# Kernel optimization log

Hardware: AMD Instinct MI355X
Metric: run time of the kernel (lower is better)

## Reference

```python
import jax, jax.numpy as jnp
import numpy as np

D_MODEL = 256
D_STATE = 64
HEADDIM = 64
EXPAND = 2
D_INNER = EXPAND * D_MODEL        # 512
D_SSM = D_INNER                   # 512
NGROUPS = 1
NHEADS = D_SSM // HEADDIM         # 8
CONV_DIM = D_SSM + 2 * NGROUPS * D_STATE   # 640
D_IN_PROJ = 2 * D_INNER + 2 * NGROUPS * D_STATE + NHEADS  # 1160
BATCH, Himg, Wimg = 8, 64, 64
EPS = 1e-5


def causal_dw_conv1d(x, w, b):
    """Depthwise causal conv1d + SiLU. x:(B,C,L), w:(C,K), b:(C,)"""
    K = w.shape[1]
    L = x.shape[-1]
    xp = jnp.pad(x, ((0, 0), (0, 0), (K - 1, 0)))
    y = b[None, :, None]
    for k in range(K):
        y = y + w[:, k][None, :, None] * xp[:, :, k:k + L]
    return jax.nn.silu(y)


def setup_inputs() -> dict:
    key = jax.random.key(0)
    ks = jax.random.split(key, 12)
    u = jax.random.normal(ks[0], (BATCH, D_MODEL, Himg, Wimg), jnp.float32)
    in_proj_w = jax.random.normal(ks[1], (D_IN_PROJ, D_MODEL), jnp.float32) * 0.02
    conv_dt_w = jax.random.normal(ks[2], (NHEADS, 4), jnp.float32) * 0.1
    # dt_bias via inverse-softplus of dt ~ logU(1e-3, 0.1) as in the module init
    dt0 = jnp.exp(jax.random.uniform(ks[3], (NHEADS,)) * (np.log(0.1) - np.log(0.001)) + np.log(0.001))
    dt_bias = dt0 + jnp.log(-jnp.expm1(-dt0))
    conv_xBC_w = jax.random.normal(ks[4], (CONV_DIM, 3), jnp.float32) * 0.1
    conv_xBC_b = jax.random.normal(ks[5], (CONV_DIM,), jnp.float32) * 0.02
    conv_z_w = jax.random.normal(ks[6], (D_SSM, 3), jnp.float32) * 0.1
    conv_z_b = jax.random.normal(ks[7], (D_SSM,), jnp.float32) * 0.02
    A_log = jnp.log(jax.random.uniform(ks[8], (NHEADS,), minval=1.0, maxval=16.0))
    D_param = jnp.ones((NHEADS,), jnp.float32)
    norm_w = jnp.ones((D_SSM,), jnp.float32)
    out_proj_w = jax.random.normal(ks[9], (D_MODEL, D_SSM, 3, 3), jnp.float32) * 0.02
    return {"u": u, "in_proj_w": in_proj_w, "conv_dt_w": conv_dt_w, "dt_bias": dt_bias,
            "conv_xBC_w": conv_xBC_w, "conv_xBC_b": conv_xBC_b,
            "conv_z_w": conv_z_w, "conv_z_b": conv_z_b,
            "A_log": A_log, "D_param": D_param, "norm_w": norm_w, "out_proj_w": out_proj_w}


def reference(u, in_proj_w, conv_dt_w, dt_bias, conv_xBC_w, conv_xBC_b,
              conv_z_w, conv_z_b, A_log, D_param, norm_w, out_proj_w):
    B, C, H, W = u.shape
    L = H * W
    # 1x1 conv in_proj -> (B, D_IN_PROJ, L)
    zxbcdt = jnp.einsum('oc,bchw->bohw', in_proj_w, u).reshape(B, D_IN_PROJ, L)
    z = zxbcdt[:, :D_SSM]                                  # (B, D_SSM, L)
    xBC = zxbcdt[:, D_SSM:D_SSM + CONV_DIM]                # (B, CONV_DIM, L)
    dt = zxbcdt[:, D_SSM + CONV_DIM:]                      # (B, NHEADS, L)

    A = -jnp.exp(A_log)                                    # (NHEADS,)
    dt = causal_dw_conv1d(dt, conv_dt_w, dt_bias)          # (B, H, L), silu'd
    xBC = causal_dw_conv1d(xBC, conv_xBC_w, conv_xBC_b)    # (B, CONV_DIM, L)

    x = xBC[:, :D_SSM]                                     # (B, D_SSM, L)
    Bm = jnp.transpose(xBC[:, D_SSM:D_SSM + D_STATE], (0, 2, 1))   # (B, L, N)
    Cm = jnp.transpose(xBC[:, D_SSM + D_STATE:], (0, 2, 1))        # (B, L, N)

    # x: (B, h*c, L) -> V: (B, h, L, c)
    V = jnp.transpose(x.reshape(B, NHEADS, HEADDIM, L), (0, 1, 3, 2))
    # dA = dt * A per head: (B, h, L, 1)
    dA = dt[:, :, :, None] * A[None, :, None, None]
    V_scaled = V * dA
    # non-causal linear attention duality (ngroups==1)
    KV = jnp.einsum('bln,bhld->bhnd', Bm, V_scaled)        # (B, h, N, d)
    y = jnp.einsum('bln,bhnd->bhld', Cm, KV) + V * D_param[None, :, None, None]
    y = jnp.transpose(y, (0, 2, 1, 3)).reshape(B, L, D_SSM)

    # gate branch
    zc = causal_dw_conv1d(z, conv_z_w, conv_z_b)           # (B, D_SSM, L)
    zc = jnp.transpose(zc, (0, 2, 1))                      # (B, L, D_SSM)
    # RMSNormGated, norm_before_gate=False: gate first then normalize
    yg = y * jax.nn.silu(zc)
    yn = yg * jax.lax.rsqrt(jnp.mean(yg * yg, axis=-1, keepdims=True) + EPS) * norm_w

    y_img = jnp.transpose(yn, (0, 2, 1)).reshape(B, D_SSM, H, W)
    out = jax.lax.conv_general_dilated(y_img, out_proj_w, (1, 1), 'SAME',
                                       dimension_numbers=('NCHW', 'OIHW', 'NCHW'))
    return out
```

## Files before the change

kernel.cpp:

```cpp
#include <hip/hip_runtime.h>
#include <math.h>


constexpr int BATCH  = 8;
constexpr int CIN    = 256;
constexpr int HH     = 64, WW = 64;
constexpr int L      = HH * WW;
constexpr int DPROJ  = 1160;
constexpr int DSSM   = 512;
constexpr int DSTATE = 64;
constexpr int NH     = 8;
constexpr int HD     = 64;
constexpr int CONVD  = 640;
constexpr int COUT   = 256;
constexpr float EPS  = 1e-5f;

typedef __attribute__((ext_vector_type(8))) short short8;
typedef __attribute__((ext_vector_type(4))) float f32x4;

static __device__ __forceinline__ float silu_f(float x) {
    return x / (1.f + __expf(-x));
}
static __device__ __forceinline__ float bf2f(unsigned short u) {
    return __uint_as_float(((unsigned)u) << 16);
}
static __device__ __forceinline__ unsigned short f2bf(float f) {
    unsigned x = __float_as_uint(f);
    unsigned r = (x + 0x7FFFu + ((x >> 16) & 1u)) >> 16;
    return (unsigned short)r;
}

static __device__ __forceinline__ void gl2lds16(const unsigned short* g, short* l) {
    __builtin_amdgcn_global_load_lds(
        (const __attribute__((address_space(1))) unsigned int*)g,
        (__attribute__((address_space(3))) unsigned int*)l, 16, 0, 0);
}

__global__ __launch_bounds__(256) void k_prep(const float* __restrict__ W,
                                              const float* __restrict__ u,
                                              const float* __restrict__ Wt,
                                              unsigned short* __restrict__ Wt2,
                                              unsigned short* __restrict__ uTt,
                                              unsigned short* __restrict__ Wb2) {
    __shared__ float Ts[32][33];
    int bx = blockIdx.x;
    int tid = threadIdx.x;

    if (bx < 160) {
        int idx8 = bx * 256 + tid;
        int tile = idx8 >> 9;
        int within = (idx8 & 511) * 8;
        int row = within >> 5;
        int slp = (within >> 3) & 3;
        int oblk = tile >> 3, ks = tile & 7;
        int o = oblk * 128 + row;
        int c = ks * 32 + (slp ^ (row & 3)) * 8;
        unsigned short s[8] = {0, 0, 0, 0, 0, 0, 0, 0};
        if (o < DPROJ) {
            float4 v0 = *(const float4*)(W + (size_t)o * CIN + c);
            float4 v1 = *(const float4*)(W + (size_t)o * CIN + c + 4);
            s[0] = f2bf(v0.x); s[1] = f2bf(v0.y); s[2] = f2bf(v0.z); s[3] = f2bf(v0.w);
            s[4] = f2bf(v1.x); s[5] = f2bf(v1.y); s[6] = f2bf(v1.z); s[7] = f2bf(v1.w);
        }
        *(uint4*)(Wt2 + (size_t)tile * 4096 + within) = *(uint4*)s;
    } else if (bx < 160 + 8192) {
        int t = bx - 160;
        int l0 = (t & 127) * 32;
        int c0 = ((t >> 7) & 7) * 32;
        int b  = t >> 10;
        {
            int r = tid >> 3, c4 = tid & 7;
            float4 v = *(const float4*)(u + ((size_t)b * CIN + c0 + r) * L + l0 + c4 * 4);
            Ts[r][c4 * 4 + 0] = v.x;
            Ts[r][c4 * 4 + 1] = v.y;
            Ts[r][c4 * 4 + 2] = v.z;
            Ts[r][c4 * 4 + 3] = v.w;
        }
        __syncthreads();
        {
            int lr = tid >> 3, cg = tid & 7;
            unsigned short s[4];
#pragma unroll
            for (int j = 0; j < 4; ++j) s[j] = f2bf(Ts[cg * 4 + j][lr]);
            int lg = l0 + lr;
            int tile = ((b * 32 + (lg >> 7)) << 3) + (c0 >> 5);
            int row = lg & 127;
            int slot = (cg >> 1) ^ (row & 3);
            size_t off = (size_t)tile * 4096 + row * 32 + slot * 8 + (cg & 1) * 4;
            *(uint2*)(uTt + off) = *(uint2*)s;
        }
    } else {
        int i = (bx - (160 + 8192)) * 256 + tid;
        int co = i >> 9, ci = i & 511;
        const float* src = Wt + (size_t)i * 9;
#pragma unroll
        for (int tap = 0; tap < 9; ++tap) {
            Wb2[(((size_t)tap * 64 + (ci >> 3)) * 256 + co) * 8 + (ci & 7)] = f2bf(src[tap]);
        }
    }
}

__global__ __launch_bounds__(256) void k_inprojm(const unsigned short* __restrict__ Wt2,
                                                 const unsigned short* __restrict__ uTt,
                                                 unsigned short* __restrict__ zx) {
    __shared__ short Ab[2][4096];
    __shared__ short Bbuf[2][4096];
    int lblk = blockIdx.x, oblk = blockIdx.y, b = blockIdx.z;
    int tid = threadIdx.x, lane = tid & 63, w = tid >> 6;
    int laneN = lane & 15, laneK = lane >> 4;

    const unsigned short* At = uTt + (size_t)(b * 32 + lblk) * 8 * 4096;
    const unsigned short* Bt = Wt2 + (size_t)oblk * 8 * 4096;

    f32x4 acc[4][4];
#pragma unroll
    for (int mt = 0; mt < 4; ++mt)
#pragma unroll
        for (int nt = 0; nt < 4; ++nt) acc[mt][nt] = (f32x4){0.f, 0.f, 0.f, 0.f};

    gl2lds16(At + tid * 8,        &Ab[0][tid * 8]);
    gl2lds16(At + 2048 + tid * 8, &Ab[0][2048 + tid * 8]);
    gl2lds16(Bt + tid * 8,        &Bbuf[0][tid * 8]);
    gl2lds16(Bt + 2048 + tid * 8, &Bbuf[0][2048 + tid * 8]);
    __syncthreads();

    int arow = (w & 1) * 64;
    int brow = (w >> 1) * 64;
    int asl = (laneK ^ (laneN & 3)) * 8;

    int cur = 0;
    for (int ks = 0; ks < 8; ++ks) {
        if (ks < 7) {
            const unsigned short* an = At + (size_t)(ks + 1) * 4096;
            const unsigned short* bn = Bt + (size_t)(ks + 1) * 4096;
            int c2 = cur ^ 1;
            gl2lds16(an + tid * 8,        &Ab[c2][tid * 8]);
            gl2lds16(an + 2048 + tid * 8, &Ab[c2][2048 + tid * 8]);
            gl2lds16(bn + tid * 8,        &Bbuf[c2][tid * 8]);
            gl2lds16(bn + 2048 + tid * 8, &Bbuf[c2][2048 + tid * 8]);
        }
        short8 av[4], bv[4];
#pragma unroll
        for (int mt = 0; mt < 4; ++mt)
            av[mt] = *(const short8*)&Ab[cur][(arow + mt * 16 + laneN) * 32 + asl];
#pragma unroll
        for (int nt = 0; nt < 4; ++nt)
            bv[nt] = *(const short8*)&Bbuf[cur][(brow + nt * 16 + laneN) * 32 + asl];
#pragma unroll
        for (int mt = 0; mt < 4; ++mt)
#pragma unroll
            for (int nt = 0; nt < 4; ++nt)
                acc[mt][nt] = __builtin_amdgcn_mfma_f32_16x16x32_bf16(av[mt], bv[nt], acc[mt][nt], 0, 0, 0);
        __syncthreads();
        cur ^= 1;
    }

    unsigned short* zb = zx + (size_t)b * DPROJ * L;
    int lbase = lblk * 128 + arow;
#pragma unroll
    for (int nt = 0; nt < 4; ++nt) {
        int o = oblk * 128 + brow + nt * 16 + laneN;
        if (o < DPROJ) {
#pragma unroll
            for (int mt = 0; mt < 4; ++mt) {
                unsigned short s[4] = {f2bf(acc[mt][nt].x), f2bf(acc[mt][nt].y),
                                       f2bf(acc[mt][nt].z), f2bf(acc[mt][nt].w)};
                *(uint2*)(zb + (size_t)o * L + lbase + mt * 16 + laneK * 4) = *(uint2*)s;
            }
        }
    }
}

__global__ __launch_bounds__(256) void k_conv1(const unsigned short* __restrict__ zx,
                                               const float* __restrict__ cw,
                                               const float* __restrict__ cb,
                                               const float* __restrict__ dw,
                                               const float* __restrict__ db,
                                               const float* __restrict__ Alog,
                                               unsigned short* __restrict__ xbc,
                                               float* __restrict__ dA) {
    int bx = blockIdx.x;
    int tid = threadIdx.x;
    if (bx < 10240) {
        int idx = bx * 256 + tid;
        int lg = idx & (L / 8 - 1);
        int c  = (idx >> 9) % CONVD;
        int b  = idx / (CONVD * (L / 8));
        int l0 = lg * 8;
        const unsigned short* row = zx + ((size_t)b * DPROJ + DSSM + c) * L;
        float x[10];
        uint4 raw = *(const uint4*)(row + l0);
        const unsigned short* s = (const unsigned short*)&raw;
#pragma unroll
        for (int t = 0; t < 8; ++t) x[2 + t] = bf2f(s[t]);
        if (l0 > 0) { x[0] = bf2f(row[l0 - 2]); x[1] = bf2f(row[l0 - 1]); }
        else        { x[0] = 0.f; x[1] = 0.f; }
        float w0 = cw[c * 3 + 0], w1 = cw[c * 3 + 1], w2 = cw[c * 3 + 2], bb = cb[c];
        uint4 o;
        unsigned short* os = (unsigned short*)&o;
#pragma unroll
        for (int t = 0; t < 8; ++t) {
            float y = bb + w0 * x[t] + w1 * x[t + 1] + w2 * x[t + 2];
            os[t] = f2bf(silu_f(y));
        }
        *(uint4*)(xbc + ((size_t)b * CONVD + c) * L + l0) = o;
    } else {
        int idx = (bx - 10240) * 256 + tid;
        int l = idx & (L - 1);
        int h = (idx >> 12) & (NH - 1);
        int b = idx >> 15;
        const unsigned short* row = zx + ((size_t)b * DPROJ + DSSM + CONVD + h) * L;
        float y = db[h];
#pragma unroll
        for (int k = 0; k < 4; ++k) {
            int ls = l + k - 3;
            if (ls >= 0) y += dw[h * 4 + k] * bf2f(row[ls]);
        }
        dA[idx] = silu_f(y) * (-__expf(Alog[h]));
    }
}

__global__ __launch_bounds__(256) void k_kvm(const unsigned short* __restrict__ xbc,
                                             const float* __restrict__ dA,
                                             float* __restrict__ pKV) {
    __shared__ float red[4][4096];
    int kc = blockIdx.x, h = blockIdx.y, b = blockIdx.z;
    int tid = threadIdx.x, lane = tid & 63, w = tid >> 6;
    int laneN = lane & 15, laneK = lane >> 4;

    const unsigned short* Bb = xbc + ((size_t)b * CONVD + DSSM) * L;
    const unsigned short* Vb = xbc + ((size_t)b * CONVD + h * HD) * L;
    const float* dAp = dA + ((size_t)b * NH + h) * L;

    f32x4 acc[4][4];
#pragma unroll
    for (int mt = 0; mt < 4; ++mt)
#pragma unroll
        for (int nt = 0; nt < 4; ++nt) acc[mt][nt] = (f32x4){0.f, 0.f, 0.f, 0.f};

    int kbase = kc * 512 + w * 128;
#pragma unroll
    for (int ks = 0; ks < 4; ++ks) {
        int kl = kbase + ks * 32 + laneK * 8;
        float4 da0 = *(const float4*)(dAp + kl);
        float4 da1 = *(const float4*)(dAp + kl + 4);
        float dav[8] = {da0.x, da0.y, da0.z, da0.w, da1.x, da1.y, da1.z, da1.w};
        short8 afr[4];
#pragma unroll
        for (int mt = 0; mt < 4; ++mt) {
            uint4 raw = *(const uint4*)(Bb + (size_t)(mt * 16 + laneN) * L + kl);
            const unsigned short* s = (const unsigned short*)&raw;
            short8 af;
#pragma unroll
            for (int j = 0; j < 8; ++j) af[j] = (short)f2bf(bf2f(s[j]) * dav[j]);
            afr[mt] = af;
        }
#pragma unroll
        for (int nt = 0; nt < 4; ++nt) {
            short8 bfr = *(const short8*)(Vb + (size_t)(nt * 16 + laneN) * L + kl);
#pragma unroll
            for (int mt = 0; mt < 4; ++mt)
                acc[mt][nt] = __builtin_amdgcn_mfma_f32_16x16x32_bf16(afr[mt], bfr, acc[mt][nt], 0, 0, 0);
        }
    }

#pragma unroll
    for (int mt = 0; mt < 4; ++mt)
#pragma unroll
        for (int nt = 0; nt < 4; ++nt)
#pragma unroll
            for (int j = 0; j < 4; ++j)
                red[w][(mt * 16 + laneK * 4 + j) * 64 + nt * 16 + laneN] = acc[mt][nt][j];
    __syncthreads();

    float* dst = pKV + (((size_t)(b * NH + h) * 8 + kc) * 4096);
#pragma unroll
    for (int q = 0; q < 4; ++q) {
        int off = q * 1024 + tid * 4;
        float4 s0 = *(const float4*)&red[0][off];
        float4 s1 = *(const float4*)&red[1][off];
        float4 s2 = *(const float4*)&red[2][off];
        float4 s3 = *(const float4*)&red[3][off];
        float4 r;
        r.x = s0.x + s1.x + s2.x + s3.x;
        r.y = s0.y + s1.y + s2.y + s3.y;
        r.z = s0.z + s1.z + s2.z + s3.z;
        r.w = s0.w + s1.w + s2.w + s3.w;
        *(float4*)(dst + off) = r;
    }
}

__global__ __launch_bounds__(256) void k_kvred(const float* __restrict__ pKV,
                                               float* __restrict__ KV) {
    int flat4 = blockIdx.x * 256 + threadIdx.x;
    int bh = flat4 >> 10;
    int nd = (flat4 & 1023) * 4;
    float4 r = make_float4(0.f, 0.f, 0.f, 0.f);
#pragma unroll
    for (int kc = 0; kc < 8; ++kc) {
        float4 v = *(const float4*)(pKV + ((size_t)bh * 8 + kc) * 4096 + nd);
        r.x += v.x; r.y += v.y; r.z += v.z; r.w += v.w;
    }
    *(float4*)(KV + (size_t)bh * 4096 + nd) = r;
}

constexpr int Y_LT = 128;

__global__ __launch_bounds__(256) void k_y5a(const unsigned short* __restrict__ xbc,
                                             const unsigned short* __restrict__ zx,
                                             const float* __restrict__ KV,
                                             const float* __restrict__ zw,
                                             const float* __restrict__ zb,
                                             const float* __restrict__ Dp,
                                             unsigned short* __restrict__ ygout) {
    __shared__ float Cs[DSTATE][Y_LT + 4];
    __shared__ float KVs[DSTATE][HD + 4];
    int l0 = blockIdx.x * Y_LT;
    int h  = blockIdx.y;
    int b  = blockIdx.z;
    int tid = threadIdx.x;
    int td = tid >> 4, tl = tid & 15;

    const unsigned short* xb = xbc + (size_t)b * CONVD * L;
#pragma unroll
    for (int j = 0; j < 4; ++j) {
        int i = j * 256 + tid;
        int nn = i >> 4, c8 = i & 15;
        uint4 raw = *(const uint4*)(xb + (size_t)(DSSM + DSTATE + nn) * L + l0 + c8 * 8);
        const unsigned short* s = (const unsigned short*)&raw;
#pragma unroll
        for (int t = 0; t < 8; ++t) Cs[nn][c8 * 8 + t] = bf2f(s[t]);
    }
    const float* kvb = KV + ((size_t)b * NH + h) * DSTATE * HD;
#pragma unroll
    for (int j = 0; j < 4; ++j) {
        int i = j * 256 + tid;
        int nn = i >> 4, d4 = i & 15;
        *(float4*)&KVs[nn][d4 * 4] = *(const float4*)(kvb + (size_t)nn * HD + d4 * 4);
    }
    __syncthreads();

    float acc[4][8];
#pragma unroll
    for (int i = 0; i < 4; ++i)
#pragma unroll
        for (int j = 0; j < 8; ++j) acc[i][j] = 0.f;

    for (int nn = 0; nn < DSTATE; ++nn) {
        float4 kv = *(const float4*)&KVs[nn][td * 4];
        float cl[8];
        *(float4*)&cl[0] = *(const float4*)&Cs[nn][tl * 8];
        *(float4*)&cl[4] = *(const float4*)&Cs[nn][tl * 8 + 4];
#pragma unroll
        for (int j = 0; j < 8; ++j) {
            acc[0][j] += kv.x * cl[j];
            acc[1][j] += kv.y * cl[j];
            acc[2][j] += kv.z * cl[j];
            acc[3][j] += kv.w * cl[j];
        }
    }

    float Dh = Dp[h];
    int lbase = l0 + tl * 8;
#pragma unroll
    for (int dj = 0; dj < 4; ++dj) {
        int c = h * HD + td * 4 + dj;
        float v[8];
        {
            uint4 raw = *(const uint4*)(xb + (size_t)c * L + lbase);
            const unsigned short* s = (const unsigned short*)&raw;
#pragma unroll
            for (int t = 0; t < 8; ++t) v[t] = bf2f(s[t]);
        }
        const unsigned short* zrow = zx + ((size_t)b * DPROJ + c) * L;
        float zv[12];
        if (lbase >= 4) {
            uint2 z0 = *(const uint2*)(zrow + lbase - 4);
            const unsigned short* s = (const unsigned short*)&z0;
#pragma unroll
            for (int t = 0; t < 4; ++t) zv[t] = bf2f(s[t]);
        } else {
            zv[0] = zv[1] = zv[2] = zv[3] = 0.f;
        }
        {
            uint4 z1 = *(const uint4*)(zrow + lbase);
            const unsigned short* s = (const unsigned short*)&z1;
#pragma unroll
            for (int t = 0; t < 8; ++t) zv[4 + t] = bf2f(s[t]);
        }
        float w0 = zw[c * 3 + 0], w1 = zw[c * 3 + 1], w2 = zw[c * 3 + 2];
        float bz = zb[c];
        uint4 pk;
        unsigned short* sp = (unsigned short*)&pk;
#pragma unroll
        for (int lj = 0; lj < 8; ++lj) {
            float y = acc[dj][lj] + v[lj] * Dh;
            float zy = bz + w0 * zv[lj + 2] + w1 * zv[lj + 3] + w2 * zv[lj + 4];
            sp[lj] = f2bf(y * silu_f(silu_f(zy)));
        }
        *(uint4*)(ygout + (size_t)b * DPROJ * L + (size_t)c * L + lbase) = pk;
    }
}

constexpr int R_LT = 32;

__global__ __launch_bounds__(256) void k_y5bT(const unsigned short* __restrict__ yg,
                                              const float* __restrict__ nw,
                                              unsigned short* __restrict__ ynT) {
    __shared__ float ygs[DSSM][R_LT + 1];
    __shared__ float red[8][R_LT];
    __shared__ float rs[R_LT];
    int l0 = blockIdx.x * R_LT;
    int b  = blockIdx.y;
    int tid = threadIdx.x;
    int ll = tid & 31, grp = tid >> 5;
    const unsigned short* ygb = yg + (size_t)b * DPROJ * L;
#pragma unroll
    for (int j = 0; j < 8; ++j) {
        int i = j * 256 + tid;
        int c = i >> 2, q = i & 3;
        uint4 raw = *(const uint4*)(ygb + (size_t)c * L + l0 + q * 8);
        const unsigned short* s = (const unsigned short*)&raw;
#pragma unroll
        for (int t = 0; t < 8; ++t) ygs[c][q * 8 + t] = bf2f(s[t]);
    }
    __syncthreads();
    float ss = 0.f;
#pragma unroll
    for (int ci = 0; ci < 64; ++ci) {
        float t = ygs[grp * 64 + ci][ll];
        ss += t * t;
    }
    red[grp][ll] = ss;
    __syncthreads();
    if (tid < R_LT) {
        float s = 0.f;
#pragma unroll
        for (int g = 0; g < 8; ++g) s += red[g][tid];
        rs[tid] = rsqrtf(s * (1.f / DSSM) + EPS);
    }
    __syncthreads();
    int lc = tid & 31, cg = tid >> 5;
    float r = rs[lc];
    unsigned short* dst = ynT + ((size_t)b * L + l0 + lc) * DSSM + cg * 64;
#pragma unroll
    for (int j = 0; j < 8; ++j) {
        uint4 pk;
        unsigned short* sp = (unsigned short*)&pk;
#pragma unroll
        for (int t = 0; t < 8; ++t) {
            int c = cg * 64 + j * 8 + t;
            sp[t] = f2bf(ygs[c][lc] * r * nw[c]);
        }
        *(uint4*)(dst + j * 8) = pk;
    }
}

__global__ __launch_bounds__(256, 4) void k_conv3m(const unsigned short* __restrict__ ynT,
                                                   const unsigned short* __restrict__ Wb2,
                                                   float* __restrict__ out) {
    __shared__ short Alds[4 * 66 * 72];
    int h0  = blockIdx.x * 2;
    int co0 = blockIdx.y * 64;
    int b   = blockIdx.z;
    int tid  = threadIdx.x;
    int lane = tid & 63;
    int wid  = tid >> 6;
    int wm = wid >> 1, wn = wid & 1;
    int laneN = lane & 15, laneK = lane >> 4;

    f32x4 acc[4][2];
#pragma unroll
    for (int mt = 0; mt < 4; ++mt)
#pragma unroll
        for (int nt = 0; nt < 2; ++nt) acc[mt][nt] = (f32x4){0.f, 0.f, 0.f, 0.f};

    const unsigned short* ynb = ynT + (size_t)b * L * DSSM;

    const int a_wi1 = tid >> 2, a_sl = tid & 3;

    if (tid < 64) {
        int rw = tid >> 3, q = tid & 7;
        int r = rw >> 1, wi = (rw & 1) ? 65 : 0;
        *(uint4*)&Alds[(r * 66 + wi) * 72 + q * 8] = make_uint4(0u, 0u, 0u, 0u);
    }

    uint4 pA[8];
#pragma unroll
    for (int j = 0; j < 4; ++j) {
        int hrow = h0 - 1 + j;
        bool ok = (hrow >= 0 && hrow < HH);
        const unsigned short* src = ynb + (size_t)(hrow * WW + a_wi1) * DSSM;
#pragma unroll
        for (int s2 = 0; s2 < 2; ++s2) {
            pA[j * 2 + s2] = make_uint4(0u, 0u, 0u, 0u);
            if (ok) pA[j * 2 + s2] = *(const uint4*)(src + (a_sl + s2 * 4) * 8);
        }
    }

    const unsigned short* wbp =
        Wb2 + ((size_t)laneK * 256 + co0 + wn * 32 + laneN) * 8;

    for (int ci0 = 0; ci0 < DSSM; ci0 += 64) {
        __syncthreads();
#pragma unroll
        for (int j = 0; j < 4; ++j)
#pragma unroll
            for (int s2 = 0; s2 < 2; ++s2)
                *(uint4*)&Alds[(j * 66 + a_wi1 + 1) * 72 + (a_sl + s2 * 4) * 8] = pA[j * 2 + s2];
        __syncthreads();

        if (ci0 + 64 < DSSM) {
            int cin = ci0 + 64;
#pragma unroll
            for (int j = 0; j < 4; ++j) {
                int hrow = h0 - 1 + j;
                bool ok = (hrow >= 0 && hrow < HH);
                const unsigned short* src = ynb + (size_t)(hrow * WW + a_wi1) * DSSM + cin;
#pragma unroll
                for (int s2 = 0; s2 < 2; ++s2) {
                    pA[j * 2 + s2] = make_uint4(0u, 0u, 0u, 0u);
                    if (ok) pA[j * 2 + s2] = *(const uint4*)(src + (a_sl + s2 * 4) * 8);
                }
            }
        }

        const unsigned short* wbc = wbp + (size_t)(ci0 >> 3) * 2048;
        short8 bC[4];
#pragma unroll
        for (int ks = 0; ks < 2; ++ks)
#pragma unroll
            for (int nt = 0; nt < 2; ++nt)
                bC[ks * 2 + nt] = *(const short8*)(wbc + (size_t)ks * 8192 + nt * 128);
#pragma unroll
        for (int tap = 0; tap < 9; ++tap) {
            short8 bN[4];
#pragma unroll
            for (int q = 0; q < 4; ++q) bN[q] = bC[q];
            if (tap < 8) {
#pragma unroll
                for (int ks = 0; ks < 2; ++ks)
#pragma unroll
                    for (int nt = 0; nt < 2; ++nt)
                        bN[ks * 2 + nt] = *(const short8*)(wbc + (size_t)(tap + 1) * 131072 +
                                                          (size_t)ks * 8192 + nt * 128);
            }
            const int kh = tap / 3, kw = tap % 3;
#pragma unroll
            for (int ks = 0; ks < 2; ++ks) {
#pragma unroll
                for (int mt = 0; mt < 4; ++mt) {
                    short8 af = *(const short8*)&Alds[((wm + kh) * 66 + laneN + mt * 16 + kw) * 72 +
                                                      (laneK + ks * 4) * 8];
                    acc[mt][0] = __builtin_amdgcn_mfma_f32_16x16x32_bf16(af, bC[ks * 2 + 0], acc[mt][0], 0, 0, 0);
                    acc[mt][1] = __builtin_amdgcn_mfma_f32_16x16x32_bf16(af, bC[ks * 2 + 1], acc[mt][1], 0, 0, 0);
                }
            }
#pragma unroll
            for (int q = 0; q < 4; ++q) bC[q] = bN[q];
        }
    }

    float* ob = out + (size_t)b * COUT * L + (size_t)(h0 + wm) * WW;
#pragma unroll
    for (int mt = 0; mt < 4; ++mt) {
#pragma unroll
        for (int nt = 0; nt < 2; ++nt) {
            int co = co0 + wn * 32 + nt * 16 + laneN;
            float4 v = make_float4(acc[mt][nt].x, acc[mt][nt].y, acc[mt][nt].z, acc[mt][nt].w);
            *(float4*)(ob + (size_t)co * L + mt * 16 + laneK * 4) = v;
        }
    }
}

extern "C" void kernel_launch(void* const* d_in, const int* in_sizes, int n_in,
                              void* d_out, int out_size, void* d_ws, size_t ws_size,
                              hipStream_t stream) {
    const float* u          = (const float*)d_in[0];
    const float* in_proj_w  = (const float*)d_in[1];
    const float* conv_dt_w  = (const float*)d_in[2];
    const float* dt_bias    = (const float*)d_in[3];
    const float* conv_xBC_w = (const float*)d_in[4];
    const float* conv_xBC_b = (const float*)d_in[5];
    const float* conv_z_w   = (const float*)d_in[6];
    const float* conv_z_b   = (const float*)d_in[7];
    const float* A_log      = (const float*)d_in[8];
    const float* D_param    = (const float*)d_in[9];
    const float* norm_w     = (const float*)d_in[10];
    const float* out_w      = (const float*)d_in[11];
    float* out = (float*)d_out;

    const size_t n_zx  = (size_t)BATCH * DPROJ * L;
    const size_t n_xbc = (size_t)BATCH * CONVD * L;
    const size_t n_yn  = (size_t)BATCH * DSSM * L;
    const size_t n_dA  = (size_t)BATCH * NH * L;
    const size_t n_KV  = (size_t)BATCH * NH * DSTATE * HD;
    const size_t n_pKV = (size_t)BATCH * NH * 8 * DSTATE * HD;
    const size_t n_Wb2 = (size_t)9 * 64 * 256 * 8;
    const size_t need  = 2 * (n_zx + n_xbc + n_yn + n_Wb2) + 4 * (n_dA + n_KV + n_pKV);
    if (ws_size < need) return;

    unsigned short* zx  = (unsigned short*)d_ws;
    unsigned short* xbc = zx + n_zx;
    unsigned short* ynT = xbc + n_xbc;
    float*          dAb = (float*)(ynT + n_yn);
    float*          KV  = dAb + n_dA;
    float*          pKV = KV + n_KV;
    unsigned short* Wb2 = (unsigned short*)(pKV + n_pKV);
    unsigned short* uTt  = ynT;
    unsigned short* Wt2  = (unsigned short*)pKV;
    unsigned short* ygbuf = zx + (size_t)DSSM * L;

    k_prep<<<8864, 256, 0, stream>>>(in_proj_w, u, out_w, Wt2, uTt, Wb2);

    dim3 g1(L / 128, 10, BATCH);
    k_inprojm<<<g1, 256, 0, stream>>>(Wt2, uTt, zx);

    k_conv1<<<11264, 256, 0, stream>>>(zx, conv_xBC_w, conv_xBC_b,
                                       conv_dt_w, dt_bias, A_log, xbc, dAb);

    dim3 g4(8, NH, BATCH);
    k_kvm<<<g4, 256, 0, stream>>>(xbc, dAb, pKV);
    k_kvred<<<256, 256, 0, stream>>>(pKV, KV);

    dim3 g5(L / Y_LT, NH, BATCH);
    k_y5a<<<g5, 256, 0, stream>>>(xbc, zx, KV, conv_z_w, conv_z_b, D_param, ygbuf);

    dim3 g5b(L / R_LT, BATCH);
    k_y5bT<<<g5b, 256, 0, stream>>>(ygbuf, norm_w, ynT);

    dim3 g6(HH / 2, COUT / 64, BATCH);
    k_conv3m<<<g6, 256, 0, stream>>>(ynT, Wb2, out);
}
```

Baseline: 238.9 us.

## Switch output 3x3 conv to 32x32x16 MFMA with 128-channel output tiles

Rewrites the final 3x3 convolution GEMM to use 32x32x16 bf16 MFMA instructions instead of 16x16x32, and doubles the output-channel tile per block from 64 to 128. The weight prep layout changes to 16-element K groups to match the new operand layout. Larger tiles halve redundant reloads of the activation halo into LDS and improve math density per LDS read. In exchange, accumulator registers grow and launch bounds drop to 2 blocks per SM, with half as many blocks in the grid.

Result: slower. 255.3 us (+6.8%).

```diff
diff --git a/kernel.cpp b/kernel.cpp
--- a/kernel.cpp
+++ b/kernel.cpp
@@ -15,8 +15,9 @@
 constexpr int COUT   = 256;
 constexpr float EPS  = 1e-5f;
 
-typedef __attribute__((ext_vector_type(8))) short short8;
-typedef __attribute__((ext_vector_type(4))) float f32x4;
+typedef __attribute__((ext_vector_type(8)))  short short8;
+typedef __attribute__((ext_vector_type(4)))  float f32x4;
+typedef __attribute__((ext_vector_type(16))) float f32x16;
 
 static __device__ __forceinline__ float silu_f(float x) {
     return x / (1.f + __expf(-x));
@@ -41,7 +42,7 @@
                                               const float* __restrict__ Wt,
                                               unsigned short* __restrict__ Wt2,
                                               unsigned short* __restrict__ uTt,
-                                              unsigned short* __restrict__ Wb2) {
+                                              unsigned short* __restrict__ Wb3) {
     __shared__ float Ts[32][33];
     int bx = blockIdx.x;
     int tid = threadIdx.x;
@@ -95,7 +96,7 @@
         const float* src = Wt + (size_t)i * 9;
 #pragma unroll
         for (int tap = 0; tap < 9; ++tap) {
-            Wb2[(((size_t)tap * 64 + (ci >> 3)) * 256 + co) * 8 + (ci & 7)] = f2bf(src[tap]);
+            Wb3[(((size_t)tap * 32 + (ci >> 4)) * 256 + co) * 16 + (ci & 15)] = f2bf(src[tap]);
         }
     }
 }
@@ -456,24 +457,26 @@
     }
 }
 
-__global__ __launch_bounds__(256, 4) void k_conv3m(const unsigned short* __restrict__ ynT,
-                                                   const unsigned short* __restrict__ Wb2,
+__global__ __launch_bounds__(256, 2) void k_conv3m(const unsigned short* __restrict__ ynT,
+                                                   const unsigned short* __restrict__ Wb3,
                                                    float* __restrict__ out) {
     __shared__ short Alds[4 * 66 * 72];
     int h0  = blockIdx.x * 2;
-    int co0 = blockIdx.y * 64;
+    int co0 = blockIdx.y * 128;
     int b   = blockIdx.z;
     int tid  = threadIdx.x;
     int lane = tid & 63;
     int wid  = tid >> 6;
     int wm = wid >> 1, wn = wid & 1;
-    int laneN = lane & 15, laneK = lane >> 4;
-
-    f32x4 acc[4][2];
-#pragma unroll
-    for (int mt = 0; mt < 4; ++mt)
-#pragma unroll
-        for (int nt = 0; nt < 2; ++nt) acc[mt][nt] = (f32x4){0.f, 0.f, 0.f, 0.f};
+    int lane32 = lane & 31, khalf = lane >> 5;
+
+    f32x16 acc[2][2];
+#pragma unroll
+    for (int mt = 0; mt < 2; ++mt)
+#pragma unroll
+        for (int nt = 0; nt < 2; ++nt)
+#pragma unroll
+            for (int q = 0; q < 16; ++q) acc[mt][nt][q] = 0.f;
 
     const unsigned short* ynb = ynT + (size_t)b * L * DSSM;
 
@@ -499,7 +502,7 @@
     }
 
     const unsigned short* wbp =
-        Wb2 + ((size_t)laneK * 256 + co0 + wn * 32 + laneN) * 8;
+        Wb3 + ((size_t)(co0 + wn * 64 + lane32) * 16) + khalf * 8;
 
     for (int ci0 = 0; ci0 < DSSM; ci0 += 64) {
         __syncthreads();
@@ -525,50 +528,59 @@
             }
         }
 
-        const unsigned short* wbc = wbp + (size_t)(ci0 >> 3) * 2048;
-        short8 bC[4];
-#pragma unroll
-        for (int ks = 0; ks < 2; ++ks)
+        const unsigned short* wbc = wbp + (size_t)(ci0 >> 4) * 4096;
+        short8 bC[2][4], bN[2][4];
+#pragma unroll
+        for (int nt = 0; nt < 2; ++nt)
+#pragma unroll
+            for (int ks = 0; ks < 4; ++ks)
+                bC[nt][ks] = *(const short8*)(wbc + (size_t)ks * 4096 + nt * 512);
+#pragma unroll
+        for (int tap = 0; tap < 9; ++tap) {
 #pragma unroll
             for (int nt = 0; nt < 2; ++nt)
-                bC[ks * 2 + nt] = *(const short8*)(wbc + (size_t)ks * 8192 + nt * 128);
-#pragma unroll
-        for (int tap = 0; tap < 9; ++tap) {
-            short8 bN[4];
-#pragma unroll
-            for (int q = 0; q < 4; ++q) bN[q] = bC[q];
+#pragma unroll
+                for (int ks = 0; ks < 4; ++ks) bN[nt][ks] = bC[nt][ks];
             if (tap < 8) {
 #pragma unroll
-                for (int ks = 0; ks < 2; ++ks)
-#pragma unroll
-                    for (int nt = 0; nt < 2; ++nt)
-                        bN[ks * 2 + nt] = *(const short8*)(wbc + (size_t)(tap + 1) * 131072 +
-                                                          (size_t)ks * 8192 + nt * 128);
+                for (int nt = 0; nt < 2; ++nt)
+#pragma unroll
+                    for (int ks = 0; ks < 4; ++ks)
+                        bN[nt][ks] = *(const short8*)(wbc + (size_t)(tap + 1) * 131072 +
+                                                     (size_t)ks * 4096 + nt * 512);
             }
             const int kh = tap / 3, kw = tap % 3;
 #pragma unroll
-            for (int ks = 0; ks < 2; ++ks) {
-#pragma unroll
-                for (int mt = 0; mt < 4; ++mt) {
-                    short8 af = *(const short8*)&Alds[((wm + kh) * 66 + laneN + mt * 16 + kw) * 72 +
-                                                      (laneK + ks * 4) * 8];
-                    acc[mt][0] = __builtin_amdgcn_mfma_f32_16x16x32_bf16(af, bC[ks * 2 + 0], acc[mt][0], 0, 0, 0);
-                    acc[mt][1] = __builtin_amdgcn_mfma_f32_16x16x32_bf16(af, bC[ks * 2 + 1], acc[mt][1], 0, 0, 0);
+            for (int ks = 0; ks < 4; ++ks) {
+#pragma unroll
+                for (int mt = 0; mt < 2; ++mt) {
+                    int wi = mt * 32 + lane32 + kw;
+                    short8 af = *(const short8*)&Alds[((wm + kh) * 66 + wi) * 72 +
+                                                      ks * 16 + khalf * 8];
+                    acc[mt][0] = __builtin_amdgcn_mfma_f32_32x32x16_bf16(af, bC[0][ks], acc[mt][0], 0, 0, 0);
+                    acc[mt][1] = __builtin_amdgcn_mfma_f32_32x32x16_bf16(af, bC[1][ks], acc[mt][1], 0, 0, 0);
                 }
             }
 #pragma unroll
-            for (int q = 0; q < 4; ++q) bC[q] = bN[q];
+            for (int nt = 0; nt < 2; ++nt)
+#pragma unroll
+                for (int ks = 0; ks < 4; ++ks) bC[nt][ks] = bN[nt][ks];
         }
     }
 
     float* ob = out + (size_t)b * COUT * L + (size_t)(h0 + wm) * WW;
 #pragma unroll
-    for (int mt = 0; mt < 4; ++mt) {
+    for (int mt = 0; mt < 2; ++mt) {
 #pragma unroll
         for (int nt = 0; nt < 2; ++nt) {
-            int co = co0 + wn * 32 + nt * 16 + laneN;
-            float4 v = make_float4(acc[mt][nt].x, acc[mt][nt].y, acc[mt][nt].z, acc[mt][nt].w);
-            *(float4*)(ob + (size_t)co * L + mt * 16 + laneK * 4) = v;
+            int co = co0 + wn * 64 + nt * 32 + lane32;
+            float* dst = ob + (size_t)co * L + mt * 32 + 4 * khalf;
+#pragma unroll
+            for (int q = 0; q < 4; ++q) {
+                float4 v = make_float4(acc[mt][nt][q * 4 + 0], acc[mt][nt][q * 4 + 1],
+                                       acc[mt][nt][q * 4 + 2], acc[mt][nt][q * 4 + 3]);
+                *(float4*)(dst + q * 8) = v;
+            }
         }
     }
 }
@@ -596,8 +608,8 @@
     const size_t n_dA  = (size_t)BATCH * NH * L;
     const size_t n_KV  = (size_t)BATCH * NH * DSTATE * HD;
     const size_t n_pKV = (size_t)BATCH * NH * 8 * DSTATE * HD;
-    const size_t n_Wb2 = (size_t)9 * 64 * 256 * 8;
-    const size_t need  = 2 * (n_zx + n_xbc + n_yn + n_Wb2) + 4 * (n_dA + n_KV + n_pKV);
+    const size_t n_Wb3 = (size_t)9 * 32 * 256 * 16;
+    const size_t need  = 2 * (n_zx + n_xbc + n_yn + n_Wb3) + 4 * (n_dA + n_KV + n_pKV);
     if (ws_size < need) return;
 
     unsigned short* zx  = (unsigned short*)d_ws;
@@ -606,12 +618,12 @@
     float*          dAb = (float*)(ynT + n_yn);
     float*          KV  = dAb + n_dA;
     float*          pKV = KV + n_KV;
-    unsigned short* Wb2 = (unsigned short*)(pKV + n_pKV);
+    unsigned short* Wb3 = (unsigned short*)(pKV + n_pKV);
     unsigned short* uTt  = ynT;
     unsigned short* Wt2  = (unsigned short*)pKV;
     unsigned short* ygbuf = zx + (size_t)DSSM * L;
 
-    k_prep<<<8864, 256, 0, stream>>>(in_proj_w, u, out_w, Wt2, uTt, Wb2);
+    k_prep<<<8864, 256, 0, stream>>>(in_proj_w, u, out_w, Wt2, uTt, Wb3);
 
     dim3 g1(L / 128, 10, BATCH);
     k_inprojm<<<g1, 256, 0, stream>>>(Wt2, uTt, zx);
@@ -629,6 +641,6 @@
     dim3 g5b(L / R_LT, BATCH);
     k_y5bT<<<g5b, 256, 0, stream>>>(ygbuf, norm_w, ynT);
 
-    dim3 g6(HH / 2, COUT / 64, BATCH);
-    k_conv3m<<<g6, 256, 0, stream>>>(ynT, Wb2, out);
-}
+    dim3 g6(HH / 2, COUT / 128, BATCH);
+    k_conv3m<<<g6, 256, 0, stream>>>(ynT, Wb3, out);
+}
```
